# Kernel optimization log

Hardware: AMD Instinct MI355X
Metric: run time of the kernel (lower is better)

## Reference

```python
import jax, jax.numpy as jnp
import numpy as np

N_NODES = 100000
N_EDGES = 1600000
D_IN = 64
D_OUT = 64


def setup_inputs() -> dict:
    key = jax.random.key(0)
    k1, k2, k3, k4, k5 = jax.random.split(key, 5)
    feat = jax.random.normal(k1, (N_NODES, D_IN), dtype=jnp.float32)
    src = jax.random.randint(k2, (N_EDGES,), 0, N_NODES, dtype=jnp.int32)
    dst = jax.random.randint(k3, (N_EDGES,), 0, N_NODES, dtype=jnp.int32)
    W = jax.random.normal(k4, (D_OUT, D_IN), dtype=jnp.float32) * (1.0 / np.sqrt(D_IN))
    b = jax.random.normal(k5, (D_OUT,), dtype=jnp.float32) * 0.01
    return {"feat": feat, "src": src, "dst": dst, "W": W, "b": b}


def reference(feat, src, dst, W, b):
    n = feat.shape[0]
    ones = jnp.ones(src.shape[0], dtype=feat.dtype)
    # out-degree normalization on source features (deg^{-1/2}, clamp min 1)
    deg_out = jnp.clip(jax.ops.segment_sum(ones, src, num_segments=n), 1.0)
    h = feat * jax.lax.rsqrt(deg_out)[:, None]  # [N, D_in]
    # copy_src + sum aggregation over edges (gather from src, scatter-add to dst)
    agg = jax.ops.segment_sum(h[src], dst, num_segments=n)  # [N, D_in]
    # dense linear
    rst = agg @ W.T + b  # [N, D_out]
    # in-degree normalization on destination
    deg_in = jnp.clip(jax.ops.segment_sum(ones, dst, num_segments=n), 1.0)
    return rst * jax.lax.rsqrt(deg_in)[:, None]
```

## Files before the change

kernel.cpp:

```cpp
#include <hip/hip_runtime.h>
#include <hip/hip_bf16.h>

#define N_NODES 100000
#define N_EDGES 1600000
#define D 64

#define NB 160
#define CH (N_EDGES / NB)
#define CH4 (CH / 4)
#define BSH 6
#define BNODES 64
#define NBUCK 1563
#define NBUCKP 1568
#define BCAP 2560

#define GK_BLOCKS 4096

#define NPART 8
#define PART_N (N_NODES / NPART)
#define TOTAL_I4 (N_EDGES / 4)
#define SCAN_BS 256
#define SCAN_ITEMS 4
#define SCAN_TILE (SCAN_BS * SCAN_ITEMS)
#define SCAN_NBLK ((N_NODES + SCAN_TILE - 1) / SCAN_TILE)

typedef unsigned short ushort8v __attribute__((ext_vector_type(8)));

__device__ __forceinline__ unsigned short f2bf_rne(float f) {
    unsigned u = __float_as_uint(f);
    u += 0x7fffu + ((u >> 16) & 1u);
    return (unsigned short)(u >> 16);
}

__global__ void __launch_bounds__(512) hist_kernel(const int* __restrict__ src,
                                                   const int* __restrict__ dst,
                                                   unsigned int* __restrict__ Hs,
                                                   unsigned int* __restrict__ Hd) {
    __shared__ unsigned hs[NBUCKP], hd[NBUCKP];
    int t = threadIdx.x;
    for (int i = t; i < NBUCKP; i += 512) { hs[i] = 0u; hd[i] = 0u; }
    __syncthreads();
    int base = blockIdx.x * CH4;
    for (int i = base + t; i < base + CH4; i += 512) {
        const int4 s4 = reinterpret_cast<const int4*>(src)[i];
        const int4 d4 = reinterpret_cast<const int4*>(dst)[i];
        atomicAdd(&hs[(unsigned)s4.x >> BSH], 1u);
        atomicAdd(&hs[(unsigned)s4.y >> BSH], 1u);
        atomicAdd(&hs[(unsigned)s4.z >> BSH], 1u);
        atomicAdd(&hs[(unsigned)s4.w >> BSH], 1u);
        atomicAdd(&hd[(unsigned)d4.x >> BSH], 1u);
        atomicAdd(&hd[(unsigned)d4.y >> BSH], 1u);
        atomicAdd(&hd[(unsigned)d4.z >> BSH], 1u);
        atomicAdd(&hd[(unsigned)d4.w >> BSH], 1u);
    }
    __syncthreads();
    unsigned int* rs = Hs + (size_t)blockIdx.x * NBUCKP;
    unsigned int* rd = Hd + (size_t)blockIdx.x * NBUCKP;
    for (int i = t; i < NBUCKP; i += 512) { rs[i] = hs[i]; rd[i] = hd[i]; }
}

__global__ void __launch_bounds__(256) colscan_kernel(unsigned int* __restrict__ H,
                                                      unsigned int* __restrict__ total) {
    __shared__ unsigned sh[256];
    int b = blockIdx.x;
    int t = threadIdx.x;
    unsigned v = (t < NB) ? H[(size_t)t * NBUCKP + b] : 0u;
    sh[t] = v;
    __syncthreads();
    for (int off = 1; off < 256; off <<= 1) {
        unsigned x = (t >= off) ? sh[t - off] : 0u;
        __syncthreads();
        sh[t] += x;
        __syncthreads();
    }
    if (t < NB) H[(size_t)t * NBUCKP + b] = sh[t] - v;
    if (t == NB - 1) total[b] = sh[t];
}

__global__ void __launch_bounds__(1024) totscan_kernel(const unsigned int* __restrict__ total_s,
                                                       unsigned int* __restrict__ cbase_s,
                                                       const unsigned int* __restrict__ total_d,
                                                       unsigned int* __restrict__ cbase_d) {
    __shared__ unsigned sh[1024];
    __shared__ unsigned carry;
    int t = threadIdx.x;
    for (int arr = 0; arr < 2; ++arr) {
        const unsigned int* tot = arr ? total_d : total_s;
        unsigned int* cb = arr ? cbase_d : cbase_s;
        if (t == 0) carry = 0u;
        __syncthreads();
        for (int chunk = 0; chunk < NBUCKP; chunk += 1024) {
            int i = chunk + t;
            unsigned v = (i < NBUCKP) ? tot[i] : 0u;
            sh[t] = v;
            __syncthreads();
            for (int off = 1; off < 1024; off <<= 1) {
                unsigned x = (t >= off) ? sh[t - off] : 0u;
                __syncthreads();
                sh[t] += x;
                __syncthreads();
            }
            unsigned c0 = carry;
            if (i < NBUCKP) cb[i] = c0 + sh[t] - v;
            __syncthreads();
            if (t == 1023) carry = c0 + sh[1023];
            __syncthreads();
        }
    }
}

__global__ void __launch_bounds__(512) scatter_kernel(const int* __restrict__ src,
                                                      const int* __restrict__ dst,
                                                      const unsigned int* __restrict__ Hs,
                                                      const unsigned int* __restrict__ Hd,
                                                      const unsigned int* __restrict__ cbase_s,
                                                      const unsigned int* __restrict__ cbase_d,
                                                      unsigned int* __restrict__ sbuck,
                                                      unsigned int* __restrict__ dbuck) {
    __shared__ unsigned cs[NBUCKP], cd[NBUCKP];
    int t = threadIdx.x;
    int blk = blockIdx.x;
    const unsigned int* rs = Hs + (size_t)blk * NBUCKP;
    const unsigned int* rd = Hd + (size_t)blk * NBUCKP;
    for (int i = t; i < NBUCKP; i += 512) {
        cs[i] = cbase_s[i] + rs[i];
        cd[i] = cbase_d[i] + rd[i];
    }
    __syncthreads();
    int base = blk * CH4;
    for (int i = base + t; i < base + CH4; i += 512) {
        const int4 s4 = reinterpret_cast<const int4*>(src)[i];
        const int4 d4 = reinterpret_cast<const int4*>(dst)[i];
        #define SCAT1(S, Dd)                                              \
            {                                                             \
                unsigned ps = atomicAdd(&cs[(unsigned)(S) >> BSH], 1u);   \
                sbuck[ps] = (unsigned)(S) & (BNODES - 1);                 \
                unsigned pd = atomicAdd(&cd[(unsigned)(Dd) >> BSH], 1u);  \
                dbuck[pd] = (((unsigned)(Dd) & (BNODES - 1)) << 17) | (unsigned)(S); \
            }
        SCAT1(s4.x, d4.x)
        SCAT1(s4.y, d4.y)
        SCAT1(s4.z, d4.z)
        SCAT1(s4.w, d4.w)
        #undef SCAT1
    }
}

__global__ void __launch_bounds__(256) degcnt_kernel(const unsigned int* __restrict__ sbuck,
                                                     const unsigned int* __restrict__ cbase_s,
                                                     const unsigned int* __restrict__ total_s,
                                                     unsigned int* __restrict__ deg_out) {
    __shared__ unsigned cnt[BNODES];
    int bk = blockIdx.x;
    int t = threadIdx.x;
    if (t < BNODES) cnt[t] = 0u;
    __syncthreads();
    unsigned base = cbase_s[bk];
    unsigned n = total_s[bk];
    for (unsigned i = t; i < n; i += 256) {
        atomicAdd(&cnt[sbuck[base + i]], 1u);
    }
    __syncthreads();
    int node = bk * BNODES + t;
    if (t < BNODES && node < N_NODES) deg_out[node] = cnt[t];
}

__global__ void __launch_bounds__(256) g_kernel(const float* __restrict__ feat,
                                                const unsigned int* __restrict__ deg_out,
                                                const float* __restrict__ W,
                                                unsigned short* __restrict__ g) {
    int t = threadIdx.x;
    int w = t >> 6;
    int lane = t & 63;

    float wreg[D];
    #pragma unroll
    for (int q = 0; q < 16; ++q) {
        const float4 t4 = *reinterpret_cast<const float4*>(&W[(size_t)lane * D + q * 4]);
        wreg[q * 4 + 0] = t4.x;
        wreg[q * 4 + 1] = t4.y;
        wreg[q * 4 + 2] = t4.z;
        wreg[q * 4 + 3] = t4.w;
    }

    for (int r = blockIdx.x * 4 + w; r < N_NODES; r += GK_BLOCKS * 4) {
        unsigned int dg = deg_out[r];
        float sc = rsqrtf((float)(dg > 0u ? dg : 1u));
        float fv = feat[(size_t)r * D + lane] * sc;
        float o = 0.f;
        #pragma unroll
        for (int k = 0; k < D; ++k) {
            float fk = __int_as_float(
                __builtin_amdgcn_readlane(__float_as_int(fv), k));
            o += fk * wreg[k];
        }
        g[(size_t)r * D + lane] = f2bf_rne(o);
    }
}

__global__ void __launch_bounds__(256) gsum_bucket(const unsigned short* __restrict__ g,
                                                   const unsigned int* __restrict__ dbuck,
                                                   const unsigned int* __restrict__ cbase_d,
                                                   const unsigned int* __restrict__ total_d,
                                                   const float* __restrict__ b,
                                                   float* __restrict__ out) {
    __shared__ int binned[BCAP];
    __shared__ unsigned cnt[BNODES], offs[BNODES], cur[BNODES];
    int bk = blockIdx.x;
    int t = threadIdx.x;
    int w = t >> 6;
    int lane = t & 63;
    int slot = lane >> 3;
    int sub  = lane & 7;

    if (t < BNODES) cnt[t] = 0u;
    __syncthreads();

    unsigned base = cbase_d[bk];
    unsigned n = total_d[bk];
    if (n > (unsigned)BCAP) n = BCAP;

    for (unsigned i = t; i < n; i += 256) {
        atomicAdd(&cnt[dbuck[base + i] >> 17], 1u);
    }
    __syncthreads();
    if (t < BNODES) offs[t] = cnt[t];
    __syncthreads();
    for (int off = 1; off < BNODES; off <<= 1) {
        unsigned x = (t < BNODES && t >= off) ? offs[t - off] : 0u;
        __syncthreads();
        if (t < BNODES) offs[t] += x;
        __syncthreads();
    }
    if (t < BNODES) cur[t] = offs[t] - cnt[t];
    __syncthreads();
    for (unsigned i = t; i < n; i += 256) {
        unsigned p = dbuck[base + i];
        unsigned d = p >> 17;
        unsigned pos = atomicAdd(&cur[d], 1u);
        binned[pos] = (int)(p & 0x1FFFFu);
    }
    __syncthreads();

    float breg = b[sub * 8 + slot];
    for (int nl = w; nl < BNODES; nl += 4) {
        int node = bk * BNODES + nl;
        if (node >= N_NODES) break;
        unsigned deg = cnt[nl];
        unsigned eoff = offs[nl] - deg;

        float acc[8];
        #pragma unroll
        for (int j = 0; j < 8; ++j) acc[j] = 0.f;

        for (unsigned b64 = 0; b64 < deg; b64 += 64u) {
            int c = (int)(deg - b64);
            if (c > 64) c = 64;
            int myidx = (lane < c) ? binned[eoff + b64 + lane] : 0;
            for (int e = 0; e < c; e += 8) {
                int es = e + slot;
                int s = __shfl(myidx, es);
                if (es < c) {
                    const ushort8v v = *reinterpret_cast<const ushort8v*>(
                        &g[(size_t)s * D + sub * 8]);
                    #pragma unroll
                    for (int j = 0; j < 8; ++j) {
                        acc[j] += __uint_as_float((unsigned)v[j] << 16);
                    }
                }
            }
        }

        #pragma unroll
        for (int j = 0; j < 8; ++j) {
            acc[j] += __shfl_xor(acc[j], 8);
            acc[j] += __shfl_xor(acc[j], 16);
            acc[j] += __shfl_xor(acc[j], 32);
        }
        float red = (slot == 0) ? acc[0] : (slot == 1) ? acc[1] :
                    (slot == 2) ? acc[2] : (slot == 3) ? acc[3] :
                    (slot == 4) ? acc[4] : (slot == 5) ? acc[5] :
                    (slot == 6) ? acc[6] : acc[7];
        int X = sub * 8 + slot;
        float rs = rsqrtf((float)(deg > 0u ? deg : 1u));
        __builtin_nontemporal_store((red + breg) * rs,
                                    out + (size_t)node * D + X);
    }
}

__global__ void __launch_bounds__(256) deg2_part(const int* __restrict__ src,
                                                 const int* __restrict__ dst,
                                                 unsigned int* __restrict__ deg_out,
                                                 unsigned int* __restrict__ deg_in) {
    int part  = blockIdx.x & (NPART - 1);
    int chunk = blockIdx.x >> 3;
    unsigned lo = (unsigned)(part * PART_N);
    int base = chunk * (TOTAL_I4 / 250);
    for (int i = base + (int)threadIdx.x; i < base + (TOTAL_I4 / 250); i += 256) {
        const int4 s4 = reinterpret_cast<const int4*>(src)[i];
        const int4 d4 = reinterpret_cast<const int4*>(dst)[i];
        if ((unsigned)(s4.x - lo) < (unsigned)PART_N) atomicAdd(&deg_out[s4.x], 1u);
        if ((unsigned)(s4.y - lo) < (unsigned)PART_N) atomicAdd(&deg_out[s4.y], 1u);
        if ((unsigned)(s4.z - lo) < (unsigned)PART_N) atomicAdd(&deg_out[s4.z], 1u);
        if ((unsigned)(s4.w - lo) < (unsigned)PART_N) atomicAdd(&deg_out[s4.w], 1u);
        if ((unsigned)(d4.x - lo) < (unsigned)PART_N) atomicAdd(&deg_in[d4.x], 1u);
        if ((unsigned)(d4.y - lo) < (unsigned)PART_N) atomicAdd(&deg_in[d4.y], 1u);
        if ((unsigned)(d4.z - lo) < (unsigned)PART_N) atomicAdd(&deg_in[d4.z], 1u);
        if ((unsigned)(d4.w - lo) < (unsigned)PART_N) atomicAdd(&deg_in[d4.w], 1u);
    }
}

__global__ void __launch_bounds__(SCAN_BS) scan1_kernel(
        const unsigned int* __restrict__ in,
        unsigned int* __restrict__ out,
        unsigned int* __restrict__ partials, int n) {
    __shared__ unsigned int ssum[SCAN_BS];
    int t = threadIdx.x;
    int base = blockIdx.x * SCAN_TILE + t * SCAN_ITEMS;
    unsigned int v[SCAN_ITEMS];
    unsigned int s = 0;
    #pragma unroll
    for (int k = 0; k < SCAN_ITEMS; ++k) {
        v[k] = (base + k < n) ? in[base + k] : 0u;
        s += v[k];
    }
    ssum[t] = s;
    __syncthreads();
    for (int off = 1; off < SCAN_BS; off <<= 1) {
        unsigned int x = (t >= off) ? ssum[t - off] : 0u;
        __syncthreads();
        ssum[t] += x;
        __syncthreads();
    }
    unsigned int excl = (t == 0) ? 0u : ssum[t - 1];
    if (t == SCAN_BS - 1) partials[blockIdx.x] = ssum[t];
    unsigned int run = excl;
    #pragma unroll
    for (int k = 0; k < SCAN_ITEMS; ++k) {
        if (base + k < n) out[base + k] = run;
        run += v[k];
    }
}

__global__ void __launch_bounds__(128) scan2_kernel(
        unsigned int* __restrict__ partials, int nb) {
    __shared__ unsigned int sh[128];
    int t = threadIdx.x;
    unsigned int v = (t < nb) ? partials[t] : 0u;
    sh[t] = v;
    __syncthreads();
    for (int off = 1; off < 128; off <<= 1) {
        unsigned int x = (t >= off) ? sh[t - off] : 0u;
        __syncthreads();
        sh[t] += x;
        __syncthreads();
    }
    if (t < nb) partials[t] = (t == 0) ? 0u : sh[t - 1];
}

__global__ void scan3_kernel(unsigned int* __restrict__ offsets,
                             const unsigned int* __restrict__ partials,
                             unsigned int* __restrict__ cursor, int n) {
    int i = blockIdx.x * blockDim.x + threadIdx.x;
    if (i < n) {
        unsigned int v = offsets[i] + partials[i / SCAN_TILE];
        offsets[i] = v;
        cursor[i]  = v;
    }
    if (i == 0) offsets[n] = N_EDGES;
}

__global__ void __launch_bounds__(256) place_part(const int* __restrict__ src,
                                                  const int* __restrict__ dst,
                                                  unsigned int* __restrict__ cursor,
                                                  int* __restrict__ sorted_src) {
    int part  = blockIdx.x & (NPART - 1);
    int chunk = blockIdx.x >> 3;
    unsigned lo = (unsigned)(part * PART_N);
    int base = chunk * (TOTAL_I4 / 250);
    for (int i = base + (int)threadIdx.x; i < base + (TOTAL_I4 / 250); i += 256) {
        const int4 s4 = reinterpret_cast<const int4*>(src)[i];
        const int4 d4 = reinterpret_cast<const int4*>(dst)[i];
        #define PLACE1(S, Dd)                                             \
            if ((unsigned)((unsigned)(Dd) - lo) < (unsigned)PART_N) {     \
                unsigned p = atomicAdd(&cursor[(Dd)], 1u);                \
                sorted_src[p] = (S);                                      \
            }
        PLACE1(s4.x, d4.x)
        PLACE1(s4.y, d4.y)
        PLACE1(s4.z, d4.z)
        PLACE1(s4.w, d4.w)
        #undef PLACE1
    }
}

__global__ void h_kernel(const float* __restrict__ feat,
                         const unsigned int* __restrict__ deg_out,
                         unsigned short* __restrict__ h) {
    int tid = blockIdx.x * blockDim.x + threadIdx.x;
    if (tid >= N_NODES * 16) return;
    int node = tid >> 4;
    unsigned int dg = deg_out[node];
    float sc = rsqrtf((float)(dg > 0u ? dg : 1u));
    const float4 v = *reinterpret_cast<const float4*>(&feat[(size_t)tid * 4]);
    ushort4 o;
    o.x = f2bf_rne(v.x * sc);
    o.y = f2bf_rne(v.y * sc);
    o.z = f2bf_rne(v.z * sc);
    o.w = f2bf_rne(v.w * sc);
    *reinterpret_cast<ushort4*>(&h[(size_t)tid * 4]) = o;
}

__global__ void __launch_bounds__(256) gg2_kernel(
        const unsigned short* __restrict__ h,
        const int* __restrict__ sorted_src,
        const unsigned int* __restrict__ offsets,
        const float* __restrict__ W,
        const float* __restrict__ b,
        float* __restrict__ out) {
    int t = threadIdx.x;
    int w = t >> 6;
    int lane = t & 63;
    int slot = lane >> 3;
    int sub  = lane & 7;

    float wreg[D];
    #pragma unroll
    for (int q = 0; q < 16; ++q) {
        const float4 t4 = *reinterpret_cast<const float4*>(&W[(size_t)lane * D + q * 4]);
        wreg[q * 4 + 0] = t4.x;
        wreg[q * 4 + 1] = t4.y;
        wreg[q * 4 + 2] = t4.z;
        wreg[q * 4 + 3] = t4.w;
    }
    float breg = b[lane];

    for (int r = blockIdx.x * 4 + w; r < N_NODES; r += GK_BLOCKS * 4) {
        unsigned int beg = offsets[r];
        unsigned int end = offsets[r + 1];
        unsigned int deg = end - beg;

        float acc[8];
        #pragma unroll
        for (int j = 0; j < 8; ++j) acc[j] = 0.f;

        for (unsigned int base = beg; base < end; base += 64u) {
            int count = (int)(end - base);
            if (count > 64) count = 64;
            int myidx = (lane < count) ? sorted_src[base + lane] : 0;
            for (int e = 0; e < count; e += 8) {
                int es = e + slot;
                int s = __shfl(myidx, es);
                if (es < count) {
                    const ushort8v v = *reinterpret_cast<const ushort8v*>(
                        &h[(size_t)s * D + sub * 8]);
                    #pragma unroll
                    for (int j = 0; j < 8; ++j) {
                        acc[j] += __uint_as_float((unsigned)v[j] << 16);
                    }
                }
            }
        }

        #pragma unroll
        for (int j = 0; j < 8; ++j) {
            acc[j] += __shfl_xor(acc[j], 8);
            acc[j] += __shfl_xor(acc[j], 16);
            acc[j] += __shfl_xor(acc[j], 32);
        }

        float o = breg;
        #pragma unroll
        for (int k = 0; k < D; ++k) {
            float av = __int_as_float(
                __builtin_amdgcn_readlane(__float_as_int(acc[k & 7]), k >> 3));
            o += av * wreg[k];
        }

        out[(size_t)r * D + lane] = o * rsqrtf((float)(deg > 0u ? deg : 1u));
    }
}

extern "C" void kernel_launch(void* const* d_in, const int* in_sizes, int n_in,
                              void* d_out, int out_size, void* d_ws, size_t ws_size,
                              hipStream_t stream) {
    const float* feat = (const float*)d_in[0];
    const int*   src  = (const int*)d_in[1];
    const int*   dst  = (const int*)d_in[2];
    const float* W    = (const float*)d_in[3];
    const float* b    = (const float*)d_in[4];
    float* out = (float*)d_out;

    {
        unsigned int* Hs      = (unsigned int*)d_ws;
        unsigned int* Hd      = Hs + (size_t)NB * NBUCKP;
        unsigned int* total_s = Hd + (size_t)NB * NBUCKP;
        unsigned int* cbase_s = total_s + NBUCKP;
        unsigned int* total_d = cbase_s + NBUCKP;
        unsigned int* cbase_d = total_d + NBUCKP;
        unsigned int* deg_out = cbase_d + NBUCKP;
        unsigned int* sbuck   = deg_out + N_NODES;
        unsigned int* dbuck   = sbuck + N_EDGES;
        unsigned short* g     = (unsigned short*)(dbuck + N_EDGES);
        size_t need_A = ((size_t)2 * NB * NBUCKP + 4 * NBUCKP + N_NODES +
                         (size_t)2 * N_EDGES + (size_t)N_NODES * D / 2) * 4;
        if (ws_size >= need_A) {
            hist_kernel<<<NB, 512, 0, stream>>>(src, dst, Hs, Hd);
            colscan_kernel<<<NBUCKP, 256, 0, stream>>>(Hs, total_s);
            colscan_kernel<<<NBUCKP, 256, 0, stream>>>(Hd, total_d);
            totscan_kernel<<<1, 1024, 0, stream>>>(total_s, cbase_s, total_d, cbase_d);
            scatter_kernel<<<NB, 512, 0, stream>>>(src, dst, Hs, Hd,
                                                   cbase_s, cbase_d, sbuck, dbuck);
            degcnt_kernel<<<NBUCK, 256, 0, stream>>>(sbuck, cbase_s, total_s, deg_out);
            g_kernel<<<GK_BLOCKS, 256, 0, stream>>>(feat, deg_out, W, g);
            gsum_bucket<<<NBUCK, 256, 0, stream>>>(g, dbuck, cbase_d, total_d, b, out);
            return;
        }
    }

    unsigned int* deg_out  = (unsigned int*)d_ws;
    unsigned int* deg_in   = deg_out + N_NODES;
    unsigned int* offsets  = deg_in + N_NODES;
    unsigned int* cursor   = offsets + N_NODES + 1;
    unsigned int* partials = cursor + N_NODES;
    size_t hdr = (size_t)(4 * N_NODES + 1 + 128);
    hdr = (hdr + 3u) & ~(size_t)3;
    int* sorted_src = (int*)d_ws + hdr;
    size_t hoff = hdr + N_EDGES;
    unsigned short* h = (unsigned short*)((unsigned int*)d_ws + hoff);

    hipMemsetAsync(d_ws, 0, (size_t)2 * N_NODES * sizeof(unsigned int), stream);
    deg2_part<<<2000, 256, 0, stream>>>(src, dst, deg_out, deg_in);
    scan1_kernel<<<SCAN_NBLK, SCAN_BS, 0, stream>>>(deg_in, offsets, partials, N_NODES);
    scan2_kernel<<<1, 128, 0, stream>>>(partials, SCAN_NBLK);
    scan3_kernel<<<(N_NODES + 255) / 256, 256, 0, stream>>>(offsets, partials, cursor, N_NODES);
    h_kernel<<<(N_NODES * 16 + 255) / 256, 256, 0, stream>>>(feat, deg_out, h);
    place_part<<<2000, 256, 0, stream>>>(src, dst, cursor, sorted_src);
    gg2_kernel<<<GK_BLOCKS, 256, 0, stream>>>(h, sorted_src, offsets, W, b, out);
}
```

Before: 159.4 us.

## Merge column-scan launches and process two nodes per wave in gather-sum

The two column-scan launches over the source and destination histograms become one launch with twice the blocks, removing a kernel launch and its serialization gap. In the bucketed gather-sum kernel, each wave now handles two destination nodes at once (nl and nl+32). Each lane loads its edge index directly from shared memory instead of broadcasting a 64-index chunk via shuffles. Keeping two independent gathers in flight is meant to raise memory-level parallelism, at the cost of more registers and idle lanes when the two nodes' degrees differ.

```diff
diff --git a/kernel.cpp b/kernel.cpp
--- a/kernel.cpp
+++ b/kernel.cpp
@@ -59,10 +59,15 @@
     for (int i = t; i < NBUCKP; i += 512) { rs[i] = hs[i]; rd[i] = hd[i]; }
 }
 
-__global__ void __launch_bounds__(256) colscan_kernel(unsigned int* __restrict__ H,
-                                                      unsigned int* __restrict__ total) {
+__global__ void __launch_bounds__(256) colscan2_kernel(unsigned int* __restrict__ Hs,
+                                                       unsigned int* __restrict__ Hd,
+                                                       unsigned int* __restrict__ total_s,
+                                                       unsigned int* __restrict__ total_d) {
     __shared__ unsigned sh[256];
-    int b = blockIdx.x;
+    int arr = (blockIdx.x >= NBUCKP) ? 1 : 0;
+    int b = blockIdx.x - arr * NBUCKP;
+    unsigned int* H     = arr ? Hd : Hs;
+    unsigned int* total = arr ? total_d : total_s;
     int t = threadIdx.x;
     unsigned v = (t < NB) ? H[(size_t)t * NBUCKP + b] : 0u;
     sh[t] = v;
@@ -243,48 +248,71 @@
     __syncthreads();
 
     float breg = b[sub * 8 + slot];
-    for (int nl = w; nl < BNODES; nl += 4) {
-        int node = bk * BNODES + nl;
-        if (node >= N_NODES) break;
-        unsigned deg = cnt[nl];
-        unsigned eoff = offs[nl] - deg;
-
-        float acc[8];
+    for (int j = 0; j < 8; ++j) {
+        int nlA = w + 4 * j;
+        int nlB = nlA + 32;
+        int nodeA = bk * BNODES + nlA;
+        int nodeB = bk * BNODES + nlB;
+        bool okA = (nodeA < N_NODES);
+        bool okB = (nodeB < N_NODES);
+        unsigned degA = okA ? cnt[nlA] : 0u;
+        unsigned degB = okB ? cnt[nlB] : 0u;
+        unsigned eoffA = okA ? (offs[nlA] - degA) : 0u;
+        unsigned eoffB = okB ? (offs[nlB] - degB) : 0u;
+        unsigned dmax = degA > degB ? degA : degB;
+
+        float accA[8], accB[8];
         #pragma unroll
-        for (int j = 0; j < 8; ++j) acc[j] = 0.f;
-
-        for (unsigned b64 = 0; b64 < deg; b64 += 64u) {
-            int c = (int)(deg - b64);
-            if (c > 64) c = 64;
-            int myidx = (lane < c) ? binned[eoff + b64 + lane] : 0;
-            for (int e = 0; e < c; e += 8) {
-                int es = e + slot;
-                int s = __shfl(myidx, es);
-                if (es < c) {
-                    const ushort8v v = *reinterpret_cast<const ushort8v*>(
-                        &g[(size_t)s * D + sub * 8]);
-                    #pragma unroll
-                    for (int j = 0; j < 8; ++j) {
-                        acc[j] += __uint_as_float((unsigned)v[j] << 16);
-                    }
-                }
+        for (int q = 0; q < 8; ++q) { accA[q] = 0.f; accB[q] = 0.f; }
+
+        for (unsigned e = 0; e < dmax; e += 8u) {
+            unsigned es = e + (unsigned)slot;
+            if (es < degA) {
+                int s = binned[eoffA + es];
+                const ushort8v v = *reinterpret_cast<const ushort8v*>(
+                    &g[(size_t)s * D + sub * 8]);
+                #pragma unroll
+                for (int q = 0; q < 8; ++q)
+                    accA[q] += __uint_as_float((unsigned)v[q] << 16);
             }
+            if (es < degB) {
+                int s = binned[eoffB + es];
+                const ushort8v v = *reinterpret_cast<const ushort8v*>(
+                    &g[(size_t)s * D + sub * 8]);
+                #pragma unroll
+                for (int q = 0; q < 8; ++q)
+                    accB[q] += __uint_as_float((unsigned)v[q] << 16);
+            }
         }
 
         #pragma unroll
-        for (int j = 0; j < 8; ++j) {
-            acc[j] += __shfl_xor(acc[j], 8);
-            acc[j] += __shfl_xor(acc[j], 16);
-            acc[j] += __shfl_xor(acc[j], 32);
-        }
-        float red = (slot == 0) ? acc[0] : (slot == 1) ? acc[1] :
-                    (slot == 2) ? acc[2] : (slot == 3) ? acc[3] :
-                    (slot == 4) ? acc[4] : (slot == 5) ? acc[5] :
-                    (slot == 6) ? acc[6] : acc[7];
+        for (int q = 0; q < 8; ++q) {
+            accA[q] += __shfl_xor(accA[q], 8);
+            accA[q] += __shfl_xor(accA[q], 16);
+            accA[q] += __shfl_xor(accA[q], 32);
+            accB[q] += __shfl_xor(accB[q], 8);
+            accB[q] += __shfl_xor(accB[q], 16);
+            accB[q] += __shfl_xor(accB[q], 32);
+        }
+        float redA = (slot == 0) ? accA[0] : (slot == 1) ? accA[1] :
+                     (slot == 2) ? accA[2] : (slot == 3) ? accA[3] :
+                     (slot == 4) ? accA[4] : (slot == 5) ? accA[5] :
+                     (slot == 6) ? accA[6] : accA[7];
+        float redB = (slot == 0) ? accB[0] : (slot == 1) ? accB[1] :
+                     (slot == 2) ? accB[2] : (slot == 3) ? accB[3] :
+                     (slot == 4) ? accB[4] : (slot == 5) ? accB[5] :
+                     (slot == 6) ? accB[6] : accB[7];
         int X = sub * 8 + slot;
-        float rs = rsqrtf((float)(deg > 0u ? deg : 1u));
-        __builtin_nontemporal_store((red + breg) * rs,
-                                    out + (size_t)node * D + X);
+        if (okA) {
+            float rs = rsqrtf((float)(degA > 0u ? degA : 1u));
+            __builtin_nontemporal_store((redA + breg) * rs,
+                                        out + (size_t)nodeA * D + X);
+        }
+        if (okB) {
+            float rs = rsqrtf((float)(degB > 0u ? degB : 1u));
+            __builtin_nontemporal_store((redB + breg) * rs,
+                                        out + (size_t)nodeB * D + X);
+        }
     }
 }
 
@@ -506,8 +534,7 @@
                          (size_t)2 * N_EDGES + (size_t)N_NODES * D / 2) * 4;
         if (ws_size >= need_A) {
             hist_kernel<<<NB, 512, 0, stream>>>(src, dst, Hs, Hd);
-            colscan_kernel<<<NBUCKP, 256, 0, stream>>>(Hs, total_s);
-            colscan_kernel<<<NBUCKP, 256, 0, stream>>>(Hd, total_d);
+            colscan2_kernel<<<2 * NBUCKP, 256, 0, stream>>>(Hs, Hd, total_s, total_d);
             totscan_kernel<<<1, 1024, 0, stream>>>(total_s, cbase_s, total_d, cbase_d);
             scatter_kernel<<<NB, 512, 0, stream>>>(src, dst, Hs, Hd,
                                                    cbase_s, cbase_d, sbuck, dbuck);
```

After: 156.4 us. About the same (-1.8%).
